# Kernel tuning notes

Measured on AMD Instinct MI355X. Metric: run time of the kernel, lower is better.

The kernel has to match this reference:

```python
import jax, jax.numpy as jnp
import numpy as np
import math

B, T, C = 4, 2048, 1024
N_HEAD = 16


def setup_inputs() -> dict:
    key = jax.random.key(0)
    k1, k2, k3 = jax.random.split(key, 3)
    x = jax.random.normal(k1, (B, T, C), dtype=jnp.float32)
    W_attn = jax.random.normal(k2, (C, 3 * C), dtype=jnp.float32) * (1.0 / math.sqrt(C))
    b_attn = jnp.zeros((3 * C,), dtype=jnp.float32)
    W_proj = jax.random.normal(k3, (C, C), dtype=jnp.float32) * (1.0 / math.sqrt(C))
    b_proj = jnp.zeros((C,), dtype=jnp.float32)
    return {"x": x, "W_attn": W_attn, "b_attn": b_attn, "W_proj": W_proj, "b_proj": b_proj}


def reference(x, W_attn, b_attn, W_proj, b_proj):
    b, t, c = x.shape
    hs = c // N_HEAD  # head size
    qkv = x @ W_attn + b_attn  # [B,T,3C]
    q, k, v = jnp.split(qkv, 3, axis=-1)
    # [B,T,C] -> [B,H,T,hs]
    q = q.reshape(b, t, N_HEAD, hs).transpose(0, 2, 1, 3)
    k = k.reshape(b, t, N_HEAD, hs).transpose(0, 2, 1, 3)
    v = v.reshape(b, t, N_HEAD, hs).transpose(0, 2, 1, 3)
    att = jnp.einsum('bhqd,bhkd->bhqk', q, k) / math.sqrt(hs)  # [B,H,T,T]
    causal = jnp.tril(jnp.ones((t, t), dtype=bool))
    att = jnp.where(causal[None, None, :, :], att, -jnp.inf)
    att = jax.nn.softmax(att, axis=-1)
    y = jnp.einsum('bhqk,bhkd->bhqd', att, v)  # [B,H,T,hs]
    y = y.transpose(0, 2, 1, 3).reshape(b, t, c)
    return y @ W_proj + b_proj
```

## Files before the change

kernel.cpp:

```cpp
#include <hip/hip_runtime.h>


typedef __bf16 bf16_t;
typedef __bf16 bf16x8 __attribute__((ext_vector_type(8)));
typedef __bf16 bf16x4 __attribute__((ext_vector_type(4)));
typedef float  f32x4  __attribute__((ext_vector_type(4)));

#define MFMA16(a, b, c) __builtin_amdgcn_mfma_f32_16x16x32_bf16((a), (b), (c), 0, 0, 0)

static __device__ __forceinline__ void gld_lds16(const bf16_t* g, void* l) {
  __builtin_amdgcn_global_load_lds(
      (const __attribute__((address_space(1))) void*)(const void*)g,
      (__attribute__((address_space(3))) void*)l, 16, 0, 0);
}

static __device__ __forceinline__ bf16x8 ldv8(const void* p) {
  return *reinterpret_cast<const bf16x8*>(p);
}

static __device__ __forceinline__ float exp2_hw(float x) {
  float r;
  asm("v_exp_f32 %0, %1" : "=v"(r) : "v"(x));
  return r;
}

__global__ __launch_bounds__(256) void prep_fused(
    const float* __restrict__ x, bf16_t* __restrict__ xb,
    const float* __restrict__ Wa, bf16_t* __restrict__ WaT,
    const float* __restrict__ Wp, bf16_t* __restrict__ WpT) {
  __shared__ float tile[32][33];
  const int bid = blockIdx.x;
  const int tid = threadIdx.x;

  if (bid < 8192) {
    const int i = bid * 256 + tid;
    float4 v = reinterpret_cast<const float4*>(x)[i];
    bf16x4 o;
    o[0] = (bf16_t)v.x; o[1] = (bf16_t)v.y; o[2] = (bf16_t)v.z; o[3] = (bf16_t)v.w;
    reinterpret_cast<bf16x4*>(xb)[i] = o;
    return;
  }
  const bool isA = bid < 11264;
  const int tb = isA ? (bid - 8192) : (bid - 11264);
  const int Nd = isA ? 3072 : 1024;
  const int nbx = isA ? 96 : 32;
  const float* in = isA ? Wa : Wp;
  bf16_t* out = isA ? WaT : WpT;
  const int n0 = (tb % nbx) * 32, k0 = (tb / nbx) * 32;
  const int tx = tid & 31, ty = tid >> 5;
#pragma unroll
  for (int i = 0; i < 4; ++i)
    tile[ty + i * 8][tx] = in[(size_t)(k0 + ty + i * 8) * Nd + (n0 + tx)];
  __syncthreads();
#pragma unroll
  for (int i = 0; i < 4; ++i)
    out[(size_t)(n0 + ty + i * 8) * 1024 + (k0 + tx)] = (bf16_t)tile[tx][ty + i * 8];
}

template <int MODE, int KD>
__global__ __launch_bounds__(256) void gemm_bf16(
    const bf16_t* __restrict__ A, const bf16_t* __restrict__ Bt,
    const float* __restrict__ bias, int M, int N,
    bf16_t* __restrict__ Qo, bf16_t* __restrict__ Ko, bf16_t* __restrict__ Vt,
    float* __restrict__ Co) {
  __shared__ alignas(16) char lds[32768];

  const int tid = threadIdx.x;
  const int wave = tid >> 6, lane = tid & 63;
  const int wm = wave >> 1, wn = wave & 1;
  const int l16 = lane & 15, kb = lane >> 4;
  const int r7 = l16 & 7;

  const int nbx = gridDim.x;
  const int lb = blockIdx.y * nbx + blockIdx.x;
  const int c = lb & 7;
  const int ii = lb >> 3;
  const int rPer = gridDim.y >> 3;
  const int tmt = c * rPer + (ii % rPer);
  const int tnt = ii / rPer;
  const int tm0 = tmt * 128, tn0 = tnt * 128;

  const int srow = wave * 8 + (lane >> 3);
  const int sp = lane & 7;

  unsigned aOff[2][4], bOff[2][4];
#pragma unroll
  for (int kc = 0; kc < 2; ++kc)
#pragma unroll
    for (int i = 0; i < 4; ++i) {
      const int rowA = wm * 64 + i * 16 + l16;
      const int rowB = wn * 64 + i * 16 + l16;
      const int slot = (kc * 4 + kb) ^ r7;
      aOff[kc][i] = rowA * 128 + slot * 16;
      bOff[kc][i] = 16384 + rowB * 128 + slot * 16;
    }

  const bf16_t* aR = A + (size_t)(tm0 + srow) * KD + sp * 8;
  const bf16_t* bR = Bt + (size_t)(tn0 + srow) * KD + sp * 8;
  const int schx = ((sp ^ (srow & 7)) - sp) * 8;

  f32x4 acc[4][4] = {};

  for (int k0 = 0; k0 < KD; k0 += 64) {
    __syncthreads();
#pragma unroll
    for (int inst = 0; inst < 4; ++inst) {
      gld_lds16(aR + (size_t)(inst * 32) * KD + k0 + schx,
                &lds[inst * 4096 + wave * 1024]);
      gld_lds16(bR + (size_t)(inst * 32) * KD + k0 + schx,
                &lds[16384 + inst * 4096 + wave * 1024]);
    }
    __syncthreads();
#pragma unroll
    for (int kc = 0; kc < 2; ++kc) {
      bf16x8 af[4], bfr[4];
#pragma unroll
      for (int mi = 0; mi < 4; ++mi) af[mi] = ldv8(&lds[aOff[kc][mi]]);
#pragma unroll
      for (int ni = 0; ni < 4; ++ni) bfr[ni] = ldv8(&lds[bOff[kc][ni]]);
#pragma unroll
      for (int mi = 0; mi < 4; ++mi)
#pragma unroll
        for (int ni = 0; ni < 4; ++ni)
          acc[mi][ni] = MFMA16(af[mi], bfr[ni], acc[mi][ni]);
    }
  }

  if constexpr (MODE == 0) {
    const int which = tn0 >> 10;
    const int bb = tm0 >> 11;
    const int t0 = (tm0 & 2047) + wm * 64 + kb * 4;
    const int hn0 = (tn0 & 1023) + wn * 64;
    const int hh = bb * 16 + (hn0 >> 6);

    if (which == 2) {
#pragma unroll
      for (int ni = 0; ni < 4; ++ni) {
        const int d = ni * 16 + l16;
        const float bv = bias[2048 + hn0 + d];
        bf16_t* p = Vt + ((size_t)hh * 64 + d) * 2048;
#pragma unroll
        for (int mi = 0; mi < 4; ++mi) {
          bf16x4 v4;
#pragma unroll
          for (int j = 0; j < 4; ++j) v4[j] = (bf16_t)(acc[mi][ni][j] + bv);
          *reinterpret_cast<bf16x4*>(&p[t0 + mi * 16]) = v4;
        }
      }
    } else {
      bf16_t* dst = which ? Ko : Qo;
      const float scl = which ? 1.0f : 0.18033688011112042f;
#pragma unroll
      for (int ni = 0; ni < 4; ++ni) {
        const int d = ni * 16 + l16;
        const float bv = bias[which * 1024 + hn0 + d];
        bf16_t* p = dst + (size_t)hh * 131072 + d;
#pragma unroll
        for (int mi = 0; mi < 4; ++mi)
#pragma unroll
          for (int j = 0; j < 4; ++j)
            p[(size_t)(t0 + mi * 16 + j) * 64] = (bf16_t)((acc[mi][ni][j] + bv) * scl);
      }
    }
  } else {
#pragma unroll
    for (int ni = 0; ni < 4; ++ni) {
      const int n = tn0 + wn * 64 + ni * 16 + l16;
      const float bv = bias[n];
#pragma unroll
      for (int mi = 0; mi < 4; ++mi) {
#pragma unroll
        for (int j = 0; j < 4; ++j) {
          const int m = tm0 + wm * 64 + mi * 16 + kb * 4 + j;
          Co[(size_t)m * N + n] = acc[mi][ni][j] + bv;
        }
      }
    }
  }
}

__global__ __launch_bounds__(512) void attn_fwd(const bf16_t* __restrict__ Qg,
                                                const bf16_t* __restrict__ Kg,
                                                const bf16_t* __restrict__ Vtg,
                                                bf16_t* __restrict__ Yg) {
  __shared__ alignas(16) char lds[49152];

  const int tid = threadIdx.x;
  const int wave = tid >> 6, lane = tid & 63;
  const int wgrp = wave >> 2;
  const int wsub = wave & 3;
  const int l16 = lane & 15, kb = lane >> 4;
  const int l8 = l16 & 7;
  const float NEG_INF = -__builtin_inff();

  const int n = blockIdx.x;
  const int bh = (n & 7) * 8 + ((n >> 3) & 7);
  const int kp = 15 - (n >> 6);
  const int qtA = kp * 2;
  const int trips = qtA + 2;
  const size_t base = (size_t)bh * (2048 * 64);
  const int b = bh >> 4, h = bh & 15;

  const int srow = tid >> 3;
  const int schunk = (tid & 7) ^ (srow & 7);
  const bf16_t* Ksrc = Kg + base + (size_t)srow * 64 + schunk * 8;
  const bf16_t* Vsrc = Vtg + base + (size_t)srow * 2048 + schunk * 8;

  auto stageK = [&](int buf, int kv0) {
    gld_lds16(Ksrc + (size_t)kv0 * 64, lds + buf * 8192 + wave * 1024);
  };
  auto stageV = [&](int buf, int kv0) {
    gld_lds16(Vsrc + kv0, lds + 16384 + buf * 8192 + wave * 1024);
  };

  const int qt = qtA + wgrp;
  const int q0 = qt * 64 + wsub * 16;
  const int q = q0 + l16;

  const bf16x8 qf0 = ldv8(Qg + base + (size_t)q * 64 + kb * 8);
  const bf16x8 qf1 = ldv8(Qg + base + (size_t)q * 64 + 32 + kb * 8);

  f32x4 o[4] = {};
  float l_r = 0.f;

  char* Pw = lds + 32768 + wave * 2048;
  const unsigned rb0 = l16 * 128 + ((kb ^ l8) * 16);
  const unsigned rb1 = l16 * 128 + (((4 + kb) ^ l8) * 16);

  stageK(0, 0);
  stageV(0, 0);
  asm volatile("s_waitcnt vmcnt(0)" ::: "memory");
  __builtin_amdgcn_s_barrier();
  __builtin_amdgcn_sched_barrier(0);

  int cur = 0;
  for (int t = 0; t < trips; ++t) {
    const int kv0 = t * 64;
    const bool more = (t + 1 < trips);
    if (more) {
      stageK(cur ^ 1, kv0 + 64);
      stageV(cur ^ 1, kv0 + 64);
    }

    if (wgrp || t <= qtA) {
      const char* k0p = lds + cur * 8192 + rb0;
      const char* k1p = lds + cur * 8192 + rb1;
      const char* v0p = lds + 16384 + cur * 8192 + rb0;
      const char* v1p = lds + 16384 + cur * 8192 + rb1;

      bf16x8 kf[8];
#pragma unroll
      for (int i = 0; i < 4; ++i) {
        kf[i * 2 + 0] = ldv8(k0p + i * 2048);
        kf[i * 2 + 1] = ldv8(k1p + i * 2048);
      }

      f32x4 s[4];
#pragma unroll
      for (int i = 0; i < 4; ++i) s[i] = f32x4{-16.f, -16.f, -16.f, -16.f};
      __builtin_amdgcn_s_setprio(1);
#pragma unroll
      for (int i = 0; i < 4; ++i) {
        s[i] = MFMA16(kf[i * 2 + 0], qf0, s[i]);
        s[i] = MFMA16(kf[i * 2 + 1], qf1, s[i]);
      }
      __builtin_amdgcn_s_setprio(0);

      bf16x8 vf[8];
#pragma unroll
      for (int i = 0; i < 4; ++i) {
        vf[i * 2 + 0] = ldv8(v0p + i * 2048);
        vf[i * 2 + 1] = ldv8(v1p + i * 2048);
      }

      if (t == qt) {
#pragma unroll
        for (int i = 0; i < 4; ++i)
#pragma unroll
          for (int j = 0; j < 4; ++j)
            if (kv0 + i * 16 + kb * 4 + j > q) s[i][j] = NEG_INF;
      }

      float ss = 0.f;
      bf16x4 pw[4];
#pragma unroll
      for (int i = 0; i < 4; ++i)
#pragma unroll
        for (int j = 0; j < 4; ++j) {
          const float p = exp2_hw(s[i][j]);
          ss += p;
          pw[i][j] = (bf16_t)p;
        }
      l_r += ss;

#pragma unroll
      for (int i = 0; i < 4; ++i) {
        const int phys = (i * 2 + (kb >> 1)) ^ l8;
        *reinterpret_cast<bf16x4*>(Pw + l16 * 128 + phys * 16 + (kb & 1) * 8) = pw[i];
      }
      const bf16x8 pb0 = ldv8(Pw + rb0);
      const bf16x8 pb1 = ldv8(Pw + rb1);

      __builtin_amdgcn_s_setprio(1);
#pragma unroll
      for (int i = 0; i < 4; ++i) {
        o[i] = MFMA16(vf[i * 2 + 0], pb0, o[i]);
        o[i] = MFMA16(vf[i * 2 + 1], pb1, o[i]);
      }
      __builtin_amdgcn_s_setprio(0);
    }

    asm volatile("s_waitcnt vmcnt(0)" ::: "memory");
    __builtin_amdgcn_s_barrier();
    __builtin_amdgcn_sched_barrier(0);
    cur ^= 1;
  }

  float lt = l_r + __shfl_xor(l_r, 16);
  lt += __shfl_xor(lt, 32);
  const float inv = 1.0f / lt;
  bf16_t* yrow = Yg + ((size_t)(b * 2048 + q)) * 1024 + h * 64;
#pragma unroll
  for (int i = 0; i < 4; ++i) {
    bf16x4 yv;
    yv[0] = (bf16_t)(o[i][0] * inv);
    yv[1] = (bf16_t)(o[i][1] * inv);
    yv[2] = (bf16_t)(o[i][2] * inv);
    yv[3] = (bf16_t)(o[i][3] * inv);
    *reinterpret_cast<bf16x4*>(yrow + i * 16 + kb * 4) = yv;
  }
}

extern "C" void kernel_launch(void* const* d_in, const int* in_sizes, int n_in,
                              void* d_out, int out_size, void* d_ws, size_t ws_size,
                              hipStream_t stream) {
  const float* x = (const float*)d_in[0];
  const float* W_attn = (const float*)d_in[1];
  const float* b_attn = (const float*)d_in[2];
  const float* W_proj = (const float*)d_in[3];
  const float* b_proj = (const float*)d_in[4];
  float* out = (float*)d_out;

  char* ws = (char*)d_ws;
  bf16_t* xb  = (bf16_t*)(ws + 0);
  bf16_t* WaT = (bf16_t*)(ws + 16777216);
  bf16_t* WpT = (bf16_t*)(ws + 23068672);
  bf16_t* Qb  = (bf16_t*)(ws + 25165824);
  bf16_t* Kb  = (bf16_t*)(ws + 41943040);
  bf16_t* Vt  = (bf16_t*)(ws + 58720256);
  bf16_t* Yb  = (bf16_t*)(ws + 75497472);

  prep_fused<<<12288, 256, 0, stream>>>(x, xb, W_attn, WaT, W_proj, WpT);

  gemm_bf16<0, 1024><<<dim3(24, 64), 256, 0, stream>>>(xb, WaT, b_attn, 8192, 3072,
                                                       Qb, Kb, Vt, nullptr);

  attn_fwd<<<1024, 512, 0, stream>>>(Qb, Kb, Vt, Yb);

  gemm_bf16<1, 1024><<<dim3(8, 64), 256, 0, stream>>>(Yb, WpT, b_proj, 8192, 1024,
                                                      nullptr, nullptr, nullptr, out);
}
```

Measured before the change: 153.6 us.

## Double-buffer B tiles in LDS and load A fragments directly to registers

The GEMM main loop now double-buffers the B tile in LDS, so the global loads for the next K-step are issued before computing on the current one. The A operand skips LDS entirely: each wave loads its MFMA fragments straight from global memory into registers, also in a ping-pong fashion. s_setprio is raised around the MFMA bursts to favour math issue. This hides load latency and cuts LDS traffic and barriers, at the cost of more VGPRs and uncoalesced, redundant global reads of A across waves that share rows.

```diff
diff --git a/kernel.cpp b/kernel.cpp
--- a/kernel.cpp
+++ b/kernel.cpp
@@ -82,48 +82,79 @@
 
   const int srow = wave * 8 + (lane >> 3);
   const int sp = lane & 7;
-
-  unsigned aOff[2][4], bOff[2][4];
-#pragma unroll
-  for (int kc = 0; kc < 2; ++kc)
-#pragma unroll
-    for (int i = 0; i < 4; ++i) {
-      const int rowA = wm * 64 + i * 16 + l16;
-      const int rowB = wn * 64 + i * 16 + l16;
-      const int slot = (kc * 4 + kb) ^ r7;
-      aOff[kc][i] = rowA * 128 + slot * 16;
-      bOff[kc][i] = 16384 + rowB * 128 + slot * 16;
-    }
-
-  const bf16_t* aR = A + (size_t)(tm0 + srow) * KD + sp * 8;
   const bf16_t* bR = Bt + (size_t)(tn0 + srow) * KD + sp * 8;
   const int schx = ((sp ^ (srow & 7)) - sp) * 8;
 
+  auto stageB = [&](int buf, int kt) {
+#pragma unroll
+    for (int inst = 0; inst < 4; ++inst)
+      gld_lds16(bR + (size_t)(inst * 32) * KD + kt * 64 + schx,
+                &lds[buf * 16384 + inst * 4096 + wave * 1024]);
+  };
+
+  unsigned bOff[2][4];
+#pragma unroll
+  for (int kc = 0; kc < 2; ++kc)
+#pragma unroll
+    for (int i = 0; i < 4; ++i) {
+      const int rowB = wn * 64 + i * 16 + l16;
+      bOff[kc][i] = rowB * 128 + (((kc * 4 + kb) ^ r7) * 16);
+    }
+
+  const bf16_t* aBase = A + (size_t)(tm0 + wm * 64 + l16) * KD + kb * 8;
+  auto loadA = [&](bf16x8 (&ar)[8], int kt) {
+#pragma unroll
+    for (int mi = 0; mi < 4; ++mi)
+#pragma unroll
+      for (int kc = 0; kc < 2; ++kc)
+        ar[mi * 2 + kc] =
+            ldv8(aBase + (size_t)kt * 64 + (size_t)(mi * 16) * KD + kc * 32);
+  };
+
   f32x4 acc[4][4] = {};
 
-  for (int k0 = 0; k0 < KD; k0 += 64) {
-    __syncthreads();
-#pragma unroll
-    for (int inst = 0; inst < 4; ++inst) {
-      gld_lds16(aR + (size_t)(inst * 32) * KD + k0 + schx,
-                &lds[inst * 4096 + wave * 1024]);
-      gld_lds16(bR + (size_t)(inst * 32) * KD + k0 + schx,
-                &lds[16384 + inst * 4096 + wave * 1024]);
-    }
-    __syncthreads();
+  auto compute = [&](const bf16x8 (&ar)[8], const char* bb) {
 #pragma unroll
     for (int kc = 0; kc < 2; ++kc) {
-      bf16x8 af[4], bfr[4];
-#pragma unroll
-      for (int mi = 0; mi < 4; ++mi) af[mi] = ldv8(&lds[aOff[kc][mi]]);
-#pragma unroll
-      for (int ni = 0; ni < 4; ++ni) bfr[ni] = ldv8(&lds[bOff[kc][ni]]);
+      bf16x8 bfr[4];
+#pragma unroll
+      for (int ni = 0; ni < 4; ++ni) bfr[ni] = ldv8(bb + bOff[kc][ni]);
+      __builtin_amdgcn_s_setprio(1);
 #pragma unroll
       for (int mi = 0; mi < 4; ++mi)
 #pragma unroll
         for (int ni = 0; ni < 4; ++ni)
-          acc[mi][ni] = MFMA16(af[mi], bfr[ni], acc[mi][ni]);
-    }
+          acc[mi][ni] = MFMA16(ar[mi * 2 + kc], bfr[ni], acc[mi][ni]);
+      __builtin_amdgcn_s_setprio(0);
+    }
+  };
+
+  constexpr int NK = KD >> 6;
+  bf16x8 aP[8], aQ[8];
+
+  stageB(0, 0);
+  loadA(aP, 0);
+  asm volatile("s_waitcnt vmcnt(0)" ::: "memory");
+  __builtin_amdgcn_s_barrier();
+  __builtin_amdgcn_sched_barrier(0);
+
+  for (int kt = 0; kt < NK; kt += 2) {
+    stageB(1, kt + 1);
+    loadA(aQ, kt + 1);
+    compute(aP, lds);
+    asm volatile("s_waitcnt vmcnt(0)" ::: "memory");
+    __builtin_amdgcn_s_barrier();
+    __builtin_amdgcn_sched_barrier(0);
+
+    const bool more = (kt + 2 < NK);
+    if (more) {
+      stageB(0, kt + 2);
+      loadA(aP, kt + 2);
+    }
+    compute(aQ, lds + 16384);
+    if (more) asm volatile("s_waitcnt vmcnt(0)" ::: "memory");
+    __builtin_amdgcn_s_barrier();
+    __builtin_amdgcn_sched_barrier(0);
   }
 
   if constexpr (MODE == 0) {
```

New measurement: 214.1 us. +39.4%, slower.
